# Kernel optimization log

Measured on AMD Instinct MI355X. Metric: run time of the kernel, lower is better.

## Reference

```python
import jax, jax.numpy as jnp
import numpy as np

N_NODES = 100000
N_EDGES = 3200000
IN_CH = 35
NUM_FAM = 26
EMBED = 8
NEW_IN = 6 + EMBED + (IN_CH - 6 - NUM_FAM)  # 17
HID = 64
LN_EPS = 1e-5


def setup_inputs() -> dict:
    key = jax.random.key(0)
    ks = jax.random.split(key, 16)
    x = jax.random.normal(ks[0], (N_NODES, IN_CH), dtype=jnp.float32)
    edge_index = jax.random.randint(ks[1], (2, N_EDGES), 0, N_NODES, dtype=jnp.int64)
    s = 0.05
    p = {
        'W_embed': jax.random.normal(ks[2], (NUM_FAM, EMBED), jnp.float32) * s,
        'b_embed': jnp.zeros((EMBED,), jnp.float32),
        'ln_g': jnp.ones((EMBED,), jnp.float32),
        'ln_b': jnp.zeros((EMBED,), jnp.float32),
        'Wl1': jax.random.normal(ks[3], (NEW_IN, HID), jnp.float32) * s,
        'bl1': jnp.zeros((HID,), jnp.float32),
        'Wr1': jax.random.normal(ks[4], (NEW_IN, HID), jnp.float32) * s,
        'Wl2': jax.random.normal(ks[5], (HID, HID), jnp.float32) * s,
        'bl2': jnp.zeros((HID,), jnp.float32),
        'Wr2': jax.random.normal(ks[6], (HID, HID), jnp.float32) * s,
        'Wl3': jax.random.normal(ks[7], (HID, HID), jnp.float32) * s,
        'bl3': jnp.zeros((HID,), jnp.float32),
        'Wr3': jax.random.normal(ks[8], (HID, HID), jnp.float32) * s,
        'Wfc': jax.random.normal(ks[9], (HID, 1), jnp.float32) * s,
        'bfc': jnp.zeros((1,), jnp.float32),
    }
    return {'x': x, 'edge_index': edge_index, **p}


def _sage(h, src, dst, Wl, bl, Wr, n):
    # PyG SAGEConv (mean aggr): lin_l(mean_{j in N(i)} h_j) + lin_r(h_i)
    msum = jax.ops.segment_sum(h[src], dst, num_segments=n)
    cnt = jax.ops.segment_sum(jnp.ones((src.shape[0],), h.dtype), dst, num_segments=n)
    mean = msum / jnp.maximum(cnt, 1.0)[:, None]
    return mean @ Wl + bl + h @ Wr


def reference(x, edge_index, W_embed, b_embed, ln_g, ln_b,
              Wl1, bl1, Wr1, Wl2, bl2, Wr2, Wl3, bl3, Wr3, Wfc, bfc):
    n = x.shape[0]
    src, dst = edge_index[0], edge_index[1]
    node_type = x[:, :6]
    onehot = x[:, 6:6 + NUM_FAM]
    other = x[:, 6 + NUM_FAM:]
    emb = onehot @ W_embed + b_embed
    mu = jnp.mean(emb, axis=-1, keepdims=True)
    var = jnp.var(emb, axis=-1, keepdims=True)
    emb = (emb - mu) * jax.lax.rsqrt(var + LN_EPS) * ln_g + ln_b
    h0 = jnp.concatenate([node_type, emb, other], axis=1)  # [N, 17]
    h1 = jax.nn.relu(_sage(h0, src, dst, Wl1, bl1, Wr1, n))
    h2 = jax.nn.relu(_sage(h1, src, dst, Wl2, bl2, Wr2, n) + h1)
    h3 = jax.nn.relu(_sage(h2, src, dst, Wl3, bl3, Wr3, n) + h2)
    return (h3 @ Wfc + bfc).squeeze(-1)
```

## Files before the change

kernel.cpp:

```cpp
#include <hip/hip_runtime.h>

#define NN 100000
#define NE 3200000
#define NB1 196
#define EPB 4096
#define NPB 782

typedef _Float16 half2v __attribute__((ext_vector_type(2)));
typedef _Float16 half8  __attribute__((ext_vector_type(8)));
typedef float    f32x4  __attribute__((ext_vector_type(4)));

__global__ __launch_bounds__(256) void k_h0(const float* __restrict__ x,
    const float* __restrict__ We, const float* __restrict__ be,
    const float* __restrict__ lg, const float* __restrict__ lb,
    _Float16* __restrict__ h0p)
{
  __shared__ float xs[256 * 35];
  int tid = threadIdx.x;
  int base_node = blockIdx.x * 256;
  int nvalid = NN - base_node; if (nvalid > 256) nvalid = 256;
  int total = nvalid * 35;
  const float* srcp = x + (size_t)base_node * 35;
  for (int j = tid; j < total; j += 256) xs[j] = srcp[j];
  __syncthreads();
  int i = base_node + tid;
  if (i >= NN) return;
  const float* xr = xs + tid * 35;
  float e[8];
  #pragma unroll
  for (int j = 0; j < 8; ++j) e[j] = be[j];
  #pragma unroll
  for (int k = 0; k < 26; ++k) {
    float o = xr[6 + k];
    #pragma unroll
    for (int j = 0; j < 8; ++j) e[j] = fmaf(o, We[k * 8 + j], e[j]);
  }
  float mu = 0.f;
  #pragma unroll
  for (int j = 0; j < 8; ++j) mu += e[j];
  mu *= 0.125f;
  float var = 0.f;
  #pragma unroll
  for (int j = 0; j < 8; ++j) { float d = e[j] - mu; var = fmaf(d, d, var); }
  var *= 0.125f;
  float rs = rsqrtf(var + 1e-5f);

  _Float16 row[32];
  #pragma unroll
  for (int j = 0; j < 6; ++j) row[j] = (_Float16)xr[j];
  #pragma unroll
  for (int j = 0; j < 8; ++j) row[6 + j] = (_Float16)((e[j] - mu) * rs * lg[j] + lb[j]);
  #pragma unroll
  for (int j = 0; j < 3; ++j) row[14 + j] = (_Float16)xr[32 + j];
  #pragma unroll
  for (int j = 17; j < 32; ++j) row[j] = (_Float16)0.f;
  half8* dst = (half8*)(h0p + (size_t)i * 32);
  #pragma unroll
  for (int q = 0; q < 4; ++q) dst[q] = *(half8*)(row + q * 8);
}

__global__ __launch_bounds__(256) void k_hist(const int* __restrict__ ei, int* __restrict__ gcur)
{
  __shared__ int hist[NB1];
  int tid = threadIdx.x;
  if (tid < NB1) hist[tid] = 0;
  __syncthreads();
  int base = blockIdx.x * EPB;
  int n = NE - base; if (n > EPB) n = EPB;
  const int* dp = ei + NE + base;
  for (int k = tid; k < n; k += 256) atomicAdd(&hist[dp[k] >> 9], 1);
  __syncthreads();
  if (tid < NB1 && hist[tid]) atomicAdd(&gcur[tid], hist[tid]);
}

__global__ __launch_bounds__(256) void k_bscan(int* __restrict__ gcur,
    int* __restrict__ bbase, int* __restrict__ row_start)
{
  __shared__ int sd[256];
  int tid = threadIdx.x;
  int v = (tid < NB1) ? gcur[tid] : 0;
  sd[tid] = v; __syncthreads();
  for (int off = 1; off < 256; off <<= 1) {
    int t = (tid >= off) ? sd[tid - off] : 0;
    __syncthreads(); sd[tid] += t; __syncthreads();
  }
  int excl = sd[tid] - v;
  if (tid < NB1) { bbase[tid] = excl; gcur[tid] = excl; }
  if (tid == 0) { bbase[NB1] = NE; row_start[NN] = NE; }
}

__global__ __launch_bounds__(256) void k_partA(const int* __restrict__ ei,
    int* __restrict__ gcur, int* __restrict__ ebuf)
{
  __shared__ int hist[NB1];
  __shared__ int lofs[NB1];
  __shared__ int gb[NB1];
  __shared__ int cur[NB1];
  __shared__ int sd[256];
  __shared__ int stage[EPB];
  __shared__ unsigned char sbkt[EPB];
  int tid = threadIdx.x;
  int base = blockIdx.x * EPB;
  int n = NE - base; if (n > EPB) n = EPB;
  if (tid < NB1) hist[tid] = 0;
  __syncthreads();
  int s[16], d[16];
  #pragma unroll
  for (int k = 0; k < 16; ++k) {
    int idx = tid + k * 256;
    if (idx < n) {
      s[k] = ei[base + idx];
      d[k] = ei[NE + base + idx];
      atomicAdd(&hist[d[k] >> 9], 1);
    } else { s[k] = -1; d[k] = 0; }
  }
  __syncthreads();
  int v = (tid < NB1) ? hist[tid] : 0;
  sd[tid] = v; __syncthreads();
  for (int off = 1; off < 256; off <<= 1) {
    int t = (tid >= off) ? sd[tid - off] : 0;
    __syncthreads(); sd[tid] += t; __syncthreads();
  }
  int excl = sd[tid] - v;
  if (tid < NB1) {
    lofs[tid] = excl; cur[tid] = excl;
    if (v) gb[tid] = atomicAdd(&gcur[tid], v);
  }
  __syncthreads();
  #pragma unroll
  for (int k = 0; k < 16; ++k) {
    if (s[k] >= 0) {
      int b = d[k] >> 9;
      int p = atomicAdd(&cur[b], 1);
      stage[p] = (s[k] << 9) | (d[k] & 511);
      sbkt[p] = (unsigned char)b;
    }
  }
  __syncthreads();
  for (int p = tid; p < n; p += 256) {
    int b = sbkt[p];
    ebuf[gb[b] + (p - lofs[b])] = stage[p];
  }
}

__global__ __launch_bounds__(512) void k_partB(const int* __restrict__ bbase,
    const int* __restrict__ ebuf, int* __restrict__ row_start, int* __restrict__ srcs)
{
  __shared__ int lcnt[512];
  __shared__ int sd[512];
  int b = blockIdx.x, tid = threadIdx.x;
  int start = bbase[b], end = bbase[b + 1];
  int n = end - start;
  lcnt[tid] = 0;
  __syncthreads();
  for (int e = tid; e < n; e += 512) atomicAdd(&lcnt[ebuf[start + e] & 511], 1);
  __syncthreads();
  int v = lcnt[tid];
  sd[tid] = v; __syncthreads();
  for (int off = 1; off < 512; off <<= 1) {
    int t = (tid >= off) ? sd[tid - off] : 0;
    __syncthreads(); sd[tid] += t; __syncthreads();
  }
  int excl = sd[tid] - v;
  int node = b * 512 + tid;
  if (node < NN) row_start[node] = start + excl;
  __syncthreads();
  lcnt[tid] = excl;
  __syncthreads();
  for (int e = tid; e < n; e += 512) {
    int w = ebuf[start + e];
    int p = atomicAdd(&lcnt[w & 511], 1);
    srcs[start + p] = w >> 9;
  }
}

template <int W>
__global__ __launch_bounds__(256) void k_agg(const _Float16* __restrict__ hin,
    const int* __restrict__ row_start, const int* __restrict__ srcs,
    _Float16* __restrict__ meanout)
{
  int wid = (blockIdx.x * 256 + threadIdx.x) >> 6;
  int lane = threadIdx.x & 63;
  if (wid >= NN) return;
  int i = __builtin_amdgcn_readfirstlane(wid);
  int rs = row_start[i], re = row_start[i + 1];
  int m = re - rs;
  constexpr int GE = (W == 32) ? 4 : 2;
  int g = (W == 32) ? (lane >> 4) : (lane >> 5);
  int f = (W == 32) ? (lane & 15) : (lane & 31);
  const int* __restrict__ sp = srcs + rs;

  float s0 = 0.f, s1 = 0.f;
  #pragma unroll 4
  for (int e = g; e < m; e += GE) {
    int src = sp[e];
    half2v v = *(const half2v*)(hin + (size_t)src * W + f * 2);
    s0 += (float)v[0];
    s1 += (float)v[1];
  }
  if (W == 32) { s0 += __shfl_xor(s0, 16); s1 += __shfl_xor(s1, 16); }
  s0 += __shfl_xor(s0, 32); s1 += __shfl_xor(s1, 32);
  float cm = fmaxf((float)m, 1.f);
  if (lane < W / 2) {
    half2v o; o[0] = (_Float16)(s0 / cm); o[1] = (_Float16)(s1 / cm);
    *(half2v*)(meanout + (size_t)i * W + lane * 2) = o;
  }
}

template <int W, int KW, bool RES, bool FINAL>
__global__ __launch_bounds__(256) void k_mlp(const _Float16* __restrict__ mean,
    const _Float16* __restrict__ h,
    const float* __restrict__ Wl, const float* __restrict__ bl,
    const float* __restrict__ Wr,
    const float* __restrict__ Wfc, const float* __restrict__ bfc,
    void* __restrict__ outp)
{
  constexpr int NKB = W / 32;
  int wave = threadIdx.x >> 6;
  int base = (blockIdx.x * 4 + wave) * 16;
  if (base >= NN) return;
  int lane = threadIdx.x & 63;
  int c = lane & 15, kg = lane >> 4;

  half8 am[NKB], ah[NKB];
  #pragma unroll
  for (int kb = 0; kb < NKB; ++kb) {
    am[kb] = *(const half8*)(mean + (size_t)(base + c) * W + kb * 32 + kg * 8);
    ah[kb] = *(const half8*)(h    + (size_t)(base + c) * W + kb * 32 + kg * 8);
  }

  half8 bwl[4][NKB], bwr[4][NKB];
  #pragma unroll
  for (int nt = 0; nt < 4; ++nt)
    #pragma unroll
    for (int kb = 0; kb < NKB; ++kb)
      #pragma unroll
      for (int j = 0; j < 8; ++j) {
        int k = kb * 32 + kg * 8 + j;
        bwl[nt][kb][j] = (k < KW) ? (_Float16)Wl[k * 64 + nt * 16 + c] : (_Float16)0.f;
        bwr[nt][kb][j] = (k < KW) ? (_Float16)Wr[k * 64 + nt * 16 + c] : (_Float16)0.f;
      }

  f32x4 acc[4] = {f32x4{0,0,0,0}, f32x4{0,0,0,0}, f32x4{0,0,0,0}, f32x4{0,0,0,0}};
  #pragma unroll
  for (int nt = 0; nt < 4; ++nt)
    #pragma unroll
    for (int kb = 0; kb < NKB; ++kb) {
      acc[nt] = __builtin_amdgcn_mfma_f32_16x16x32_f16(am[kb], bwl[nt][kb], acc[nt], 0, 0, 0);
      acc[nt] = __builtin_amdgcn_mfma_f32_16x16x32_f16(ah[kb], bwr[nt][kb], acc[nt], 0, 0, 0);
    }

  if (!FINAL) {
    _Float16* hout = (_Float16*)outp;
    #pragma unroll
    for (int nt = 0; nt < 4; ++nt) {
      float bia = bl[nt * 16 + c];
      #pragma unroll
      for (int r = 0; r < 4; ++r) {
        int node = base + kg * 4 + r;
        float v = acc[nt][r] + bia;
        if (RES) v += (float)h[(size_t)node * 64 + nt * 16 + c];
        v = fmaxf(v, 0.f);
        hout[(size_t)node * 64 + nt * 16 + c] = (_Float16)v;
      }
    }
  } else {
    float wf = Wfc[0];
    (void)wf;
    #pragma unroll
    for (int r = 0; r < 4; ++r) {
      float p = 0.f;
      #pragma unroll
      for (int nt = 0; nt < 4; ++nt) {
        float v = acc[nt][r] + bl[nt * 16 + c];
        if (RES) v += (float)h[(size_t)(base + kg * 4 + r) * 64 + nt * 16 + c];
        v = fmaxf(v, 0.f);
        p = fmaf(v, Wfc[nt * 16 + c], p);
      }
      p += __shfl_xor(p, 1); p += __shfl_xor(p, 2);
      p += __shfl_xor(p, 4); p += __shfl_xor(p, 8);
      if (c == 0) ((float*)outp)[base + kg * 4 + r] = p + bfc[0];
    }
  }
}

extern "C" void kernel_launch(void* const* d_in, const int* in_sizes, int n_in,
                              void* d_out, int out_size, void* d_ws, size_t ws_size,
                              hipStream_t stream)
{
  const float* x   = (const float*)d_in[0];
  const int*   ei  = (const int*)d_in[1];
  const float* We  = (const float*)d_in[2];
  const float* be  = (const float*)d_in[3];
  const float* lg  = (const float*)d_in[4];
  const float* lb  = (const float*)d_in[5];
  const float* Wl1 = (const float*)d_in[6];
  const float* bl1 = (const float*)d_in[7];
  const float* Wr1 = (const float*)d_in[8];
  const float* Wl2 = (const float*)d_in[9];
  const float* bl2 = (const float*)d_in[10];
  const float* Wr2 = (const float*)d_in[11];
  const float* Wl3 = (const float*)d_in[12];
  const float* bl3 = (const float*)d_in[13];
  const float* Wr3 = (const float*)d_in[14];
  const float* Wfc = (const float*)d_in[15];
  const float* bfc = (const float*)d_in[16];
  (void)in_sizes; (void)n_in; (void)out_size; (void)ws_size;

  size_t off = 0;
  auto carve = [&](size_t bytes) -> void* {
    void* p = (char*)d_ws + off;
    off += (bytes + 255) & ~(size_t)255;
    return p;
  };
  _Float16* h0p    = (_Float16*)carve((size_t)NN * 32 * 2);
  _Float16* mean1  = (_Float16*)carve((size_t)NN * 32 * 2);
  char*     uni    = (char*)carve((size_t)NE * 4);
  int*      ebuf   = (int*)uni;
  _Float16* h1     = (_Float16*)uni;
  _Float16* mean23 = (_Float16*)carve((size_t)NN * 64 * 2);
  _Float16* h2     = (_Float16*)carve((size_t)NN * 64 * 2);
  int*      row_start = (int*)carve((size_t)(NN + 1) * 4);
  int*      srcs   = (int*)carve((size_t)NE * 4);
  int*      gcur   = (int*)carve((size_t)NB1 * 4);
  int*      bbase  = (int*)carve((size_t)(NB1 + 1) * 4);

  const int nblk_node = (NN + 255) / 256;
  const int nblk_wave = (NN + 3) / 4;
  const int nblk_mlp  = (NN + 63) / 64;

  hipMemsetAsync(gcur, 0, (size_t)NB1 * 4, stream);
  k_h0<<<nblk_node, 256, 0, stream>>>(x, We, be, lg, lb, h0p);
  k_hist<<<NPB, 256, 0, stream>>>(ei, gcur);
  k_bscan<<<1, 256, 0, stream>>>(gcur, bbase, row_start);
  k_partA<<<NPB, 256, 0, stream>>>(ei, gcur, ebuf);
  k_partB<<<NB1, 512, 0, stream>>>(bbase, ebuf, row_start, srcs);

  k_agg<32><<<nblk_wave, 256, 0, stream>>>(h0p, row_start, srcs, mean1);
  k_mlp<32, 17, false, false><<<nblk_mlp, 256, 0, stream>>>(mean1, h0p, Wl1, bl1, Wr1, nullptr, nullptr, h1);
  k_agg<64><<<nblk_wave, 256, 0, stream>>>(h1, row_start, srcs, mean23);
  k_mlp<64, 64, true, false><<<nblk_mlp, 256, 0, stream>>>(mean23, h1, Wl2, bl2, Wr2, nullptr, nullptr, h2);
  k_agg<64><<<nblk_wave, 256, 0, stream>>>(h2, row_start, srcs, mean23);
  k_mlp<64, 64, true, true><<<nblk_mlp, 256, 0, stream>>>(mean23, h2, Wl3, bl3, Wr3, Wfc, bfc, d_out);
}
```

Baseline: 426.5 us.

## Stage MLP weights in LDS, process 4 tiles per wave, widen agg loads

```diff
diff --git a/kernel.cpp b/kernel.cpp
--- a/kernel.cpp
+++ b/kernel.cpp
@@ -7,6 +7,7 @@
 #define NPB 782
 
 typedef _Float16 half2v __attribute__((ext_vector_type(2)));
+typedef _Float16 half4  __attribute__((ext_vector_type(4)));
 typedef _Float16 half8  __attribute__((ext_vector_type(8)));
 typedef float    f32x4  __attribute__((ext_vector_type(4)));
 
@@ -179,31 +180,46 @@
     const int* __restrict__ row_start, const int* __restrict__ srcs,
     _Float16* __restrict__ meanout)
 {
+  constexpr int FP = W / 16;
   int wid = (blockIdx.x * 256 + threadIdx.x) >> 6;
   int lane = threadIdx.x & 63;
   if (wid >= NN) return;
   int i = __builtin_amdgcn_readfirstlane(wid);
   int rs = row_start[i], re = row_start[i + 1];
   int m = re - rs;
-  constexpr int GE = (W == 32) ? 4 : 2;
-  int g = (W == 32) ? (lane >> 4) : (lane >> 5);
-  int f = (W == 32) ? (lane & 15) : (lane & 31);
+  int g = lane >> 4;
+  int f = lane & 15;
   const int* __restrict__ sp = srcs + rs;
 
-  float s0 = 0.f, s1 = 0.f;
+  float acc[FP];
+  #pragma unroll
+  for (int q = 0; q < FP; ++q) acc[q] = 0.f;
+
   #pragma unroll 4
-  for (int e = g; e < m; e += GE) {
+  for (int e = g; e < m; e += 4) {
     int src = sp[e];
-    half2v v = *(const half2v*)(hin + (size_t)src * W + f * 2);
-    s0 += (float)v[0];
-    s1 += (float)v[1];
-  }
-  if (W == 32) { s0 += __shfl_xor(s0, 16); s1 += __shfl_xor(s1, 16); }
-  s0 += __shfl_xor(s0, 32); s1 += __shfl_xor(s1, 32);
+    if (W == 64) {
+      half4 v = *(const half4*)(hin + (size_t)src * 64 + f * 4);
+      #pragma unroll
+      for (int q = 0; q < 4; ++q) acc[q] += (float)v[q];
+    } else {
+      half2v v = *(const half2v*)(hin + (size_t)src * 32 + f * 2);
+      acc[0] += (float)v[0];
+      acc[1] += (float)v[1];
+    }
+  }
+  #pragma unroll
+  for (int q = 0; q < FP; ++q) {
+    acc[q] += __shfl_xor(acc[q], 16);
+    acc[q] += __shfl_xor(acc[q], 32);
+  }
   float cm = fmaxf((float)m, 1.f);
-  if (lane < W / 2) {
-    half2v o; o[0] = (_Float16)(s0 / cm); o[1] = (_Float16)(s1 / cm);
-    *(half2v*)(meanout + (size_t)i * W + lane * 2) = o;
+  if (lane < 16) {
+    _Float16 o[FP];
+    #pragma unroll
+    for (int q = 0; q < FP; ++q) o[q] = (_Float16)(acc[q] / cm);
+    if (W == 64) *(half4*)(meanout + (size_t)i * 64 + f * 4) = *(half4*)o;
+    else         *(half2v*)(meanout + (size_t)i * 32 + f * 2) = *(half2v*)o;
   }
 }
 
@@ -215,71 +231,75 @@
     const float* __restrict__ Wfc, const float* __restrict__ bfc,
     void* __restrict__ outp)
 {
+  __shared__ _Float16 lwl[64 * W];
+  __shared__ _Float16 lwr[64 * W];
+  int tid = threadIdx.x;
+  for (int idx = tid; idx < 64 * W; idx += 256) {
+    int nn = idx / W, kk = idx % W;
+    lwl[idx] = (kk < KW) ? (_Float16)Wl[kk * 64 + nn] : (_Float16)0.f;
+    lwr[idx] = (kk < KW) ? (_Float16)Wr[kk * 64 + nn] : (_Float16)0.f;
+  }
+  __syncthreads();
   constexpr int NKB = W / 32;
-  int wave = threadIdx.x >> 6;
-  int base = (blockIdx.x * 4 + wave) * 16;
-  if (base >= NN) return;
-  int lane = threadIdx.x & 63;
+  int wv = tid >> 6, lane = tid & 63;
   int c = lane & 15, kg = lane >> 4;
 
-  half8 am[NKB], ah[NKB];
-  #pragma unroll
-  for (int kb = 0; kb < NKB; ++kb) {
-    am[kb] = *(const half8*)(mean + (size_t)(base + c) * W + kb * 32 + kg * 8);
-    ah[kb] = *(const half8*)(h    + (size_t)(base + c) * W + kb * 32 + kg * 8);
-  }
-
   half8 bwl[4][NKB], bwr[4][NKB];
   #pragma unroll
   for (int nt = 0; nt < 4; ++nt)
     #pragma unroll
-    for (int kb = 0; kb < NKB; ++kb)
+    for (int kb = 0; kb < NKB; ++kb) {
+      bwl[nt][kb] = *(const half8*)&lwl[(nt * 16 + c) * W + kb * 32 + kg * 8];
+      bwr[nt][kb] = *(const half8*)&lwr[(nt * 16 + c) * W + kb * 32 + kg * 8];
+    }
+
+  int wavebase = blockIdx.x * 256 + wv * 64;
+  #pragma unroll
+  for (int ti = 0; ti < 4; ++ti) {
+    int tbase = wavebase + ti * 16;
+    if (tbase >= NN) break;
+    half8 am[NKB], ah[NKB];
+    #pragma unroll
+    for (int kb = 0; kb < NKB; ++kb) {
+      am[kb] = *(const half8*)(mean + (size_t)(tbase + c) * W + kb * 32 + kg * 8);
+      ah[kb] = *(const half8*)(h    + (size_t)(tbase + c) * W + kb * 32 + kg * 8);
+    }
+    f32x4 acc[4] = {f32x4{0,0,0,0}, f32x4{0,0,0,0}, f32x4{0,0,0,0}, f32x4{0,0,0,0}};
+    #pragma unroll
+    for (int nt = 0; nt < 4; ++nt)
       #pragma unroll
-      for (int j = 0; j < 8; ++j) {
-        int k = kb * 32 + kg * 8 + j;
-        bwl[nt][kb][j] = (k < KW) ? (_Float16)Wl[k * 64 + nt * 16 + c] : (_Float16)0.f;
-        bwr[nt][kb][j] = (k < KW) ? (_Float16)Wr[k * 64 + nt * 16 + c] : (_Float16)0.f;
+      for (int kb = 0; kb < NKB; ++kb) {
+        acc[nt] = __builtin_amdgcn_mfma_f32_16x16x32_f16(am[kb], bwl[nt][kb], acc[nt], 0, 0, 0);
+        acc[nt] = __builtin_amdgcn_mfma_f32_16x16x32_f16(ah[kb], bwr[nt][kb], acc[nt], 0, 0, 0);
       }
-
-  f32x4 acc[4] = {f32x4{0,0,0,0}, f32x4{0,0,0,0}, f32x4{0,0,0,0}, f32x4{0,0,0,0}};
-  #pragma unroll
-  for (int nt = 0; nt < 4; ++nt)
-    #pragma unroll
-    for (int kb = 0; kb < NKB; ++kb) {
-      acc[nt] = __builtin_amdgcn_mfma_f32_16x16x32_f16(am[kb], bwl[nt][kb], acc[nt], 0, 0, 0);
-      acc[nt] = __builtin_amdgcn_mfma_f32_16x16x32_f16(ah[kb], bwr[nt][kb], acc[nt], 0, 0, 0);
-    }
-
-  if (!FINAL) {
-    _Float16* hout = (_Float16*)outp;
-    #pragma unroll
-    for (int nt = 0; nt < 4; ++nt) {
-      float bia = bl[nt * 16 + c];
+    if (!FINAL) {
+      _Float16* hout = (_Float16*)outp;
+      #pragma unroll
+      for (int nt = 0; nt < 4; ++nt) {
+        float bia = bl[nt * 16 + c];
+        #pragma unroll
+        for (int r = 0; r < 4; ++r) {
+          int node = tbase + kg * 4 + r;
+          float v = acc[nt][r] + bia;
+          if (RES) v += (float)h[(size_t)node * 64 + nt * 16 + c];
+          hout[(size_t)node * 64 + nt * 16 + c] = (_Float16)fmaxf(v, 0.f);
+        }
+      }
+    } else {
       #pragma unroll
       for (int r = 0; r < 4; ++r) {
-        int node = base + kg * 4 + r;
-        float v = acc[nt][r] + bia;
-        if (RES) v += (float)h[(size_t)node * 64 + nt * 16 + c];
-        v = fmaxf(v, 0.f);
-        hout[(size_t)node * 64 + nt * 16 + c] = (_Float16)v;
+        float p = 0.f;
+        #pragma unroll
+        for (int nt = 0; nt < 4; ++nt) {
+          float v = acc[nt][r] + bl[nt * 16 + c];
+          if (RES) v += (float)h[(size_t)(tbase + kg * 4 + r) * 64 + nt * 16 + c];
+          v = fmaxf(v, 0.f);
+          p = fmaf(v, Wfc[nt * 16 + c], p);
+        }
+        p += __shfl_xor(p, 1); p += __shfl_xor(p, 2);
+        p += __shfl_xor(p, 4); p += __shfl_xor(p, 8);
+        if (c == 0) ((float*)outp)[tbase + kg * 4 + r] = p + bfc[0];
       }
-    }
-  } else {
-    float wf = Wfc[0];
-    (void)wf;
-    #pragma unroll
-    for (int r = 0; r < 4; ++r) {
-      float p = 0.f;
-      #pragma unroll
-      for (int nt = 0; nt < 4; ++nt) {
-        float v = acc[nt][r] + bl[nt * 16 + c];
-        if (RES) v += (float)h[(size_t)(base + kg * 4 + r) * 64 + nt * 16 + c];
-        v = fmaxf(v, 0.f);
-        p = fmaf(v, Wfc[nt * 16 + c], p);
-      }
-      p += __shfl_xor(p, 1); p += __shfl_xor(p, 2);
-      p += __shfl_xor(p, 4); p += __shfl_xor(p, 8);
-      if (c == 0) ((float*)outp)[base + kg * 4 + r] = p + bfc[0];
     }
   }
 }
@@ -327,7 +347,6 @@
 
   const int nblk_node = (NN + 255) / 256;
   const int nblk_wave = (NN + 3) / 4;
-  const int nblk_mlp  = (NN + 63) / 64;
 
   hipMemsetAsync(gcur, 0, (size_t)NB1 * 4, stream);
   k_h0<<<nblk_node, 256, 0, stream>>>(x, We, be, lg, lb, h0p);
@@ -337,9 +356,9 @@
   k_partB<<<NB1, 512, 0, stream>>>(bbase, ebuf, row_start, srcs);
 
   k_agg<32><<<nblk_wave, 256, 0, stream>>>(h0p, row_start, srcs, mean1);
-  k_mlp<32, 17, false, false><<<nblk_mlp, 256, 0, stream>>>(mean1, h0p, Wl1, bl1, Wr1, nullptr, nullptr, h1);
+  k_mlp<32, 17, false, false><<<nblk_node, 256, 0, stream>>>(mean1, h0p, Wl1, bl1, Wr1, nullptr, nullptr, h1);
   k_agg<64><<<nblk_wave, 256, 0, stream>>>(h1, row_start, srcs, mean23);
-  k_mlp<64, 64, true, false><<<nblk_mlp, 256, 0, stream>>>(mean23, h1, Wl2, bl2, Wr2, nullptr, nullptr, h2);
+  k_mlp<64, 64, true, false><<<nblk_node, 256, 0, stream>>>(mean23, h1, Wl2, bl2, Wr2, nullptr, nullptr, h2);
   k_agg<64><<<nblk_wave, 256, 0, stream>>>(h2, row_start, srcs, mean23);
-  k_mlp<64, 64, true, true><<<nblk_mlp, 256, 0, stream>>>(mean23, h2, Wl3, bl3, Wr3, Wfc, bfc, d_out);
-}
+  k_mlp<64, 64, true, true><<<nblk_node, 256, 0, stream>>>(mean23, h2, Wl3, bl3, Wr3, Wfc, bfc, d_out);
+}
```

Measured after the change: 398.9 us. -6.5%, faster.
